# Kernel tuning notes

Measured on AMD Instinct MI355X. Metric: run time of the kernel, lower is better.

## Reference

```python
import jax, jax.numpy as jnp
import numpy as np

N_NODES = 100000

def gcn_layer(x, W, b, src, dst, norm):
    # x: [N, Fin], W: [Fin, Fout]; fused linear then normalized neighbor aggregation
    h = x @ W                                   # [N, Fout]
    msg = h[src] * norm[:, None]                # gather + per-edge scale, [E', Fout]
    agg = jax.ops.segment_sum(msg, dst, num_segments=N_NODES)  # scatter-add
    return agg + b

def _add_self_loops_and_norm(edge_index):
    src, dst = edge_index[0], edge_index[1]
    loop = jnp.arange(N_NODES, dtype=src.dtype)
    src = jnp.concatenate([src, loop])
    dst = jnp.concatenate([dst, loop])
    deg = jax.ops.segment_sum(jnp.ones_like(dst, dtype=jnp.float32), dst, num_segments=N_NODES)
    dis = jnp.where(deg > 0, jax.lax.rsqrt(deg), 0.0)   # deg^{-1/2}
    norm = dis[src] * dis[dst]                          # symmetric GCN normalization
    return src, dst, norm

def setup_inputs() -> dict:
    key = jax.random.key(0)
    k1, k2, k3, k4, k5, k6 = jax.random.split(key, 6)
    F_IN, F_HID, F_OUT = 64, 64, 64
    E = 1600000
    x = jax.random.normal(k1, (N_NODES, F_IN), dtype=jnp.float32)
    edge_index = jax.random.randint(k2, (2, E), 0, N_NODES, dtype=jnp.int64)
    s1 = 1.0 / np.sqrt(F_IN)
    s2 = 1.0 / np.sqrt(F_HID)
    W1 = jax.random.uniform(k3, (F_IN, F_HID), dtype=jnp.float32, minval=-s1, maxval=s1)
    b1 = jax.random.uniform(k4, (F_HID,), dtype=jnp.float32, minval=-s1, maxval=s1)
    W2 = jax.random.uniform(k5, (F_HID, F_OUT), dtype=jnp.float32, minval=-s2, maxval=s2)
    b2 = jax.random.uniform(k6, (F_OUT,), dtype=jnp.float32, minval=-s2, maxval=s2)
    return {"x": x, "edge_index": edge_index, "W1": W1, "b1": b1, "W2": W2, "b2": b2}

def reference(x, edge_index, W1, b1, W2, b2):
    src, dst, norm = _add_self_loops_and_norm(edge_index)
    h = gcn_layer(x, W1, b1, src, dst, norm)
    h = jax.nn.relu(h)
    h = gcn_layer(h, W2, b2, src, dst, norm)
    return h
```

## Files before the change

### kernel.cpp

```cpp
#include <hip/hip_runtime.h>
#include <cstdint>
#include <cstddef>


#define BK_SHIFT 9
#define BK_NODES 512
#define EPB 8192
#define CAP 12288
#define NBMAX 256

typedef short bf16x8 __attribute__((ext_vector_type(8)));
typedef float f32x4  __attribute__((ext_vector_type(4)));

static __device__ __forceinline__ unsigned short f2b(float f) {
    unsigned x = __float_as_uint(f);
    unsigned r = (x + 0x7FFFu + ((x >> 16) & 1u)) >> 16;
    return (unsigned short)r;
}
static __device__ __forceinline__ float blo(unsigned u) {
    return __uint_as_float(u << 16);
}
static __device__ __forceinline__ float bhi(unsigned u) {
    return __uint_as_float(u & 0xFFFF0000u);
}
static __device__ __forceinline__ void splitbf(float x, short& hi, short& lo) {
    unsigned short h = f2b(x);
    hi = (short)h;
    float r = x - __uint_as_float((unsigned)h << 16);
    lo = (short)f2b(r);
}

__global__ void k_init(int* __restrict__ gcursor, int NB) {
    int t = threadIdx.x;
    if (t < NB) gcursor[t] = t * CAP;
}

__global__ void __launch_bounds__(256) k_bscatter(const int* __restrict__ src,
                                                  const int* __restrict__ dst,
                                                  int* __restrict__ gcursor,
                                                  unsigned* __restrict__ packed,
                                                  int E, int NB) {
    __shared__ int hist[NBMAX];
    __shared__ int base[NBMAX];
    int t = threadIdx.x;
    for (int i = t; i < NB; i += 256) hist[i] = 0;
    __syncthreads();
    int e0 = blockIdx.x * EPB;
    int e1 = min(e0 + EPB, E);
    int4 dv[8];
    int kd[8];
#pragma unroll
    for (int k = 0; k < 8; ++k) {
        int e = e0 + t * 4 + k * 1024;
        kd[k] = (e + 3 < e1) ? 1 : 0;
        if (kd[k]) dv[k] = *(const int4*)(dst + e);
    }
#pragma unroll
    for (int k = 0; k < 8; ++k) {
        if (kd[k]) {
            atomicAdd(&hist[dv[k].x >> BK_SHIFT], 1);
            atomicAdd(&hist[dv[k].y >> BK_SHIFT], 1);
            atomicAdd(&hist[dv[k].z >> BK_SHIFT], 1);
            atomicAdd(&hist[dv[k].w >> BK_SHIFT], 1);
        }
    }
    __syncthreads();
    for (int i = t; i < NB; i += 256) {
        int c = hist[i];
        base[i] = c ? atomicAdd(&gcursor[i], c) : 0;
        hist[i] = 0;
    }
    __syncthreads();
    int4 sv[8];
#pragma unroll
    for (int k = 0; k < 8; ++k) {
        int e = e0 + t * 4 + k * 1024;
        if (kd[k]) sv[k] = *(const int4*)(src + e);
    }
#pragma unroll
    for (int k = 0; k < 8; ++k) {
        if (kd[k]) {
            int b0 = dv[k].x >> BK_SHIFT;
            int p0 = base[b0] + atomicAdd(&hist[b0], 1);
            packed[p0] = (unsigned)sv[k].x | (((unsigned)dv[k].x & (BK_NODES - 1)) << 17);
            int b1 = dv[k].y >> BK_SHIFT;
            int p1 = base[b1] + atomicAdd(&hist[b1], 1);
            packed[p1] = (unsigned)sv[k].y | (((unsigned)dv[k].y & (BK_NODES - 1)) << 17);
            int b2 = dv[k].z >> BK_SHIFT;
            int p2 = base[b2] + atomicAdd(&hist[b2], 1);
            packed[p2] = (unsigned)sv[k].z | (((unsigned)dv[k].z & (BK_NODES - 1)) << 17);
            int b3 = dv[k].w >> BK_SHIFT;
            int p3 = base[b3] + atomicAdd(&hist[b3], 1);
            packed[p3] = (unsigned)sv[k].w | (((unsigned)dv[k].w & (BK_NODES - 1)) << 17);
        }
    }
}

__global__ void __launch_bounds__(512) k_build(const unsigned* __restrict__ packed,
                                               const int* __restrict__ gcursor,
                                               int* __restrict__ rp,
                                               int* __restrict__ dega,
                                               float* __restrict__ dis,
                                               int* __restrict__ col, int N) {
    __shared__ int cnt_s[BK_NODES];
    __shared__ int tmp[BK_NODES];
    int b = blockIdx.x;
    int t = threadIdx.x;
    int node0 = b << BK_SHIFT;
    int nnode = min(BK_NODES, N - node0);
    int e0 = b * CAP;
    int e1 = gcursor[b];
    cnt_s[t] = 0;
    __syncthreads();
    for (int e = e0 + t * 4; e < e1; e += 2048) {
        int m = e1 - e; m = m > 4 ? 4 : m;
        unsigned p0 = packed[e];
        unsigned p1 = (m > 1) ? packed[e + 1] : 0;
        unsigned p2 = (m > 2) ? packed[e + 2] : 0;
        unsigned p3 = (m > 3) ? packed[e + 3] : 0;
        atomicAdd(&cnt_s[p0 >> 17], 1);
        if (m > 1) atomicAdd(&cnt_s[p1 >> 17], 1);
        if (m > 2) atomicAdd(&cnt_s[p2 >> 17], 1);
        if (m > 3) atomicAdd(&cnt_s[p3 >> 17], 1);
    }
    __syncthreads();
    int v = cnt_s[t];
    tmp[t] = v;
    __syncthreads();
    for (int off = 1; off < BK_NODES; off <<= 1) {
        int a = (t >= off) ? tmp[t - off] : 0;
        __syncthreads();
        tmp[t] += a;
        __syncthreads();
    }
    int excl = tmp[t] - v;
    if (t < nnode) {
        rp[node0 + t] = e0 + excl;
        dega[node0 + t] = v;
        dis[node0 + t] = rsqrtf((float)(v + 1));
    }
    __syncthreads();
    cnt_s[t] = excl;
    __syncthreads();
    for (int e = e0 + t * 4; e < e1; e += 2048) {
        int m = e1 - e; m = m > 4 ? 4 : m;
        unsigned p0 = packed[e];
        unsigned p1 = (m > 1) ? packed[e + 1] : 0;
        unsigned p2 = (m > 2) ? packed[e + 2] : 0;
        unsigned p3 = (m > 3) ? packed[e + 3] : 0;
        int pos0 = atomicAdd(&cnt_s[p0 >> 17], 1);
        col[e0 + pos0] = (int)(p0 & 0x1FFFFu);
        if (m > 1) { int pos = atomicAdd(&cnt_s[p1 >> 17], 1); col[e0 + pos] = (int)(p1 & 0x1FFFFu); }
        if (m > 2) { int pos = atomicAdd(&cnt_s[p2 >> 17], 1); col[e0 + pos] = (int)(p2 & 0x1FFFFu); }
        if (m > 3) { int pos = atomicAdd(&cnt_s[p3 >> 17], 1); col[e0 + pos] = (int)(p3 & 0x1FFFFu); }
    }
}

__global__ void __launch_bounds__(256) k_gemm_mfma(const float* __restrict__ X,
                                                   const float* __restrict__ W,
                                                   const float* __restrict__ dis,
                                                   unsigned short* __restrict__ g16,
                                                   int n, int nstrips) {
    __shared__ float Ws[4096];
    int t = threadIdx.x;
    {
        const float4* W4 = (const float4*)W;
        float4* S4 = (float4*)Ws;
#pragma unroll
        for (int i = 0; i < 4; ++i) S4[t + i * 256] = W4[t + i * 256];
    }
    __syncthreads();
    int wid  = t >> 6;
    int lane = t & 63;
    int quad = lane >> 4;
    int fl   = lane & 15;

    bf16x8 Bh[4][2], Bl[4][2];
#pragma unroll
    for (int tt = 0; tt < 4; ++tt)
#pragma unroll
        for (int c = 0; c < 2; ++c)
#pragma unroll
            for (int j = 0; j < 8; ++j) {
                float w = Ws[(c * 32 + quad * 8 + j) * 64 + tt * 16 + fl];
                short hi, lo;
                splitbf(w, hi, lo);
                Bh[tt][c][j] = hi;
                Bl[tt][c][j] = lo;
            }

    for (int s = blockIdx.x * 4 + wid; s < nstrips; s += gridDim.x * 4) {
        int row0 = s << 4;
        const float4* xp = (const float4*)(X + ((size_t)(row0 + fl) << 6));
        bf16x8 Ah[2], Al[2];
#pragma unroll
        for (int c = 0; c < 2; ++c) {
            float4 a = xp[c * 8 + quad * 2];
            float4 b = xp[c * 8 + quad * 2 + 1];
            float xs[8] = {a.x, a.y, a.z, a.w, b.x, b.y, b.z, b.w};
#pragma unroll
            for (int j = 0; j < 8; ++j) {
                short hi, lo;
                splitbf(xs[j], hi, lo);
                Ah[c][j] = hi;
                Al[c][j] = lo;
            }
        }
        f32x4 acc[4];
#pragma unroll
        for (int tt = 0; tt < 4; ++tt) acc[tt] = (f32x4){0.f, 0.f, 0.f, 0.f};
#pragma unroll
        for (int tt = 0; tt < 4; ++tt) {
#pragma unroll
            for (int c = 0; c < 2; ++c) {
                acc[tt] = __builtin_amdgcn_mfma_f32_16x16x32_bf16(Ah[c], Bh[tt][c], acc[tt], 0, 0, 0);
                acc[tt] = __builtin_amdgcn_mfma_f32_16x16x32_bf16(Al[c], Bh[tt][c], acc[tt], 0, 0, 0);
                acc[tt] = __builtin_amdgcn_mfma_f32_16x16x32_bf16(Ah[c], Bl[tt][c], acc[tt], 0, 0, 0);
            }
        }
        float4 dv = *(const float4*)(dis + row0 + quad * 4);
        float ds4[4] = {dv.x, dv.y, dv.z, dv.w};
#pragma unroll
        for (int tt = 0; tt < 4; ++tt) {
#pragma unroll
            for (int r = 0; r < 4; ++r) {
                int row = row0 + quad * 4 + r;
                float v = acc[tt][r] * ds4[r];
                g16[(size_t)row * 64 + tt * 16 + fl] = f2b(v);
            }
        }
    }
}

template <int RELU>
__global__ void __launch_bounds__(256) k_agg(const unsigned short* __restrict__ g16,
                                             const int* __restrict__ col,
                                             const int* __restrict__ rp,
                                             const int* __restrict__ dega,
                                             const float* __restrict__ dis,
                                             const float* __restrict__ bias,
                                             float* __restrict__ out, int n) {
    int lane = threadIdx.x & 63;
    int wv = (blockIdx.x << 2) | (threadIdx.x >> 6);
    int sub = lane >> 3;
    int fl  = lane & 7;
    int base = wv << 3;
    if (base >= n) return;
    int node = base + sub;
    int nd = min(node, n - 1);
    int start = rp[nd];
    int deg = (node < n) ? dega[nd] : 0;
    int dm = max(deg, __shfl_xor(deg, 8));
    dm = max(dm, __shfl_xor(dm, 16));
    dm = max(dm, __shfl_xor(dm, 32));

    uint4 us = *((const uint4*)(g16 + ((size_t)nd << 6)) + fl);
    float A[8], B[8], C[8], D[8];
    A[0] = blo(us.x); A[1] = bhi(us.x); A[2] = blo(us.y); A[3] = bhi(us.y);
    A[4] = blo(us.z); A[5] = bhi(us.z); A[6] = blo(us.w); A[7] = bhi(us.w);
#pragma unroll
    for (int j = 0; j < 8; ++j) { B[j] = 0.f; C[j] = 0.f; D[j] = 0.f; }

    int sb = sub << 3;
    for (int c = 0; c < dm; c += 8) {
        int rem = deg - c;
        int cv = 0;
        if (fl < rem) cv = col[start + c + fl];
        int rr[8];
#pragma unroll
        for (int i = 0; i < 8; ++i) rr[i] = __shfl(cv, sb + i);
        uint4 u[8];
#pragma unroll
        for (int i = 0; i < 8; ++i)
            if (i < rem) u[i] = *((const uint4*)(g16 + ((size_t)rr[i] << 6)) + fl);
#pragma unroll
        for (int i = 0; i < 8; ++i) {
            if (i < rem) {
                float* T = ((i & 3) == 0) ? A : ((i & 3) == 1) ? B : ((i & 3) == 2) ? C : D;
                T[0] += blo(u[i].x); T[1] += bhi(u[i].x);
                T[2] += blo(u[i].y); T[3] += bhi(u[i].y);
                T[4] += blo(u[i].z); T[5] += bhi(u[i].z);
                T[6] += blo(u[i].w); T[7] += bhi(u[i].w);
            }
        }
    }
    float s = dis[nd];
    float4 bv0 = ((const float4*)bias)[fl * 2];
    float4 bv1 = ((const float4*)bias)[fl * 2 + 1];
    float r[8];
#pragma unroll
    for (int j = 0; j < 8; ++j) r[j] = (A[j] + B[j]) + (C[j] + D[j]);
    float4 o0, o1;
    o0.x = fmaf(s, r[0], bv0.x); o0.y = fmaf(s, r[1], bv0.y);
    o0.z = fmaf(s, r[2], bv0.z); o0.w = fmaf(s, r[3], bv0.w);
    o1.x = fmaf(s, r[4], bv1.x); o1.y = fmaf(s, r[5], bv1.y);
    o1.z = fmaf(s, r[6], bv1.z); o1.w = fmaf(s, r[7], bv1.w);
    if (RELU) {
        o0.x = fmaxf(o0.x, 0.f); o0.y = fmaxf(o0.y, 0.f);
        o0.z = fmaxf(o0.z, 0.f); o0.w = fmaxf(o0.w, 0.f);
        o1.x = fmaxf(o1.x, 0.f); o1.y = fmaxf(o1.y, 0.f);
        o1.z = fmaxf(o1.z, 0.f); o1.w = fmaxf(o1.w, 0.f);
    }
    if (node < n) {
        float4* op = (float4*)(out + ((size_t)node << 6)) + fl * 2;
        op[0] = o0;
        op[1] = o1;
    }
}

extern "C" void kernel_launch(void* const* d_in, const int* in_sizes, int n_in,
                              void* d_out, int out_size, void* d_ws, size_t ws_size,
                              hipStream_t stream) {
    const float* x  = (const float*)d_in[0];
    const int*   ei = (const int*)d_in[1];
    const float* W1 = (const float*)d_in[2];
    const float* b1 = (const float*)d_in[3];
    const float* W2 = (const float*)d_in[4];
    const float* b2 = (const float*)d_in[5];
    float* out = (float*)d_out;

    const int N = in_sizes[0] / 64;
    const int E = in_sizes[1] / 2;
    const int NB = (N + BK_NODES - 1) >> BK_SHIFT;
    const int nstrips = (N + 15) >> 4;
    const int* src = ei;
    const int* dst = ei + E;

    char* ws = (char*)d_ws;
    size_t off = 0;
    auto alloc = [&](size_t bytes) -> void* {
        void* p = ws + off;
        off = (off + bytes + 255) & ~(size_t)255;
        return p;
    };
    int*            gcursor = (int*)alloc((size_t)NB * 4);
    int*            rp      = (int*)alloc((size_t)N * 4);
    int*            dega    = (int*)alloc((size_t)N * 4);
    float*          dis     = (float*)alloc((size_t)N * 4);
    unsigned*       packed  = (unsigned*)alloc((size_t)NB * CAP * 4);
    int*            col     = (int*)alloc((size_t)NB * CAP * 4);
    unsigned short* g16     = (unsigned short*)alloc((size_t)N * 64 * 2);
    float*          h       = (float*)alloc((size_t)N * 64 * 4);
    (void)ws_size;

    k_init<<<1, 256, 0, stream>>>(gcursor, NB);
    k_bscatter<<<(E + EPB - 1) / EPB, 256, 0, stream>>>(src, dst, gcursor, packed, E, NB);
    k_build<<<NB, 512, 0, stream>>>(packed, gcursor, rp, dega, dis, col, N);

    k_gemm_mfma<<<782, 256, 0, stream>>>(x, W1, dis, g16, N, nstrips);
    k_agg<1><<<(N + 31) / 32, 256, 0, stream>>>(g16, col, rp, dega, dis, b1, h, N);
    k_gemm_mfma<<<782, 256, 0, stream>>>(h, W2, dis, g16, N, nstrips);
    k_agg<0><<<(N + 31) / 32, 256, 0, stream>>>(g16, col, rp, dega, dis, b2, out, N);
}
```

Measured before the change: 205.2 us.

## Fuse layer-1 aggregation with layer-2 linear transform in one kernel

Adds a kernel that aggregates layer-1 neighbor features, applies bias and ReLU, then multiplies by W2 held in shared memory using wavefront shuffles. It writes the bf16 layer-2 features directly, removing the fp32 hidden buffer round-trip and one kernel launch. In exchange, the MFMA GEMM for layer 2 becomes scalar FMA work with 64 shuffles per node, which adds ALU and latency cost to the aggregation kernel.

```diff
diff --git a/kernel.cpp b/kernel.cpp
--- a/kernel.cpp
+++ b/kernel.cpp
@@ -308,6 +308,116 @@
     }
 }
 
+__global__ void __launch_bounds__(256) k_agg_gemm(const unsigned short* __restrict__ g16,
+                                                  const int* __restrict__ col,
+                                                  const int* __restrict__ rp,
+                                                  const int* __restrict__ dega,
+                                                  const float* __restrict__ dis,
+                                                  const float* __restrict__ bias,
+                                                  const float* __restrict__ W2,
+                                                  unsigned short* __restrict__ g16out,
+                                                  int n) {
+    __shared__ float W2s[4096];
+    int t = threadIdx.x;
+    {
+        const float4* W4 = (const float4*)W2;
+        float4* S4 = (float4*)W2s;
+#pragma unroll
+        for (int i = 0; i < 4; ++i) S4[t + i * 256] = W4[t + i * 256];
+    }
+    __syncthreads();
+
+    int lane = t & 63;
+    int wv = (blockIdx.x << 2) | (t >> 6);
+    int sub = lane >> 3;
+    int fl  = lane & 7;
+    int base = wv << 3;
+    if (base >= n) return;
+    int node = base + sub;
+    int nd = min(node, n - 1);
+    int start = rp[nd];
+    int deg = (node < n) ? dega[nd] : 0;
+    int dm = max(deg, __shfl_xor(deg, 8));
+    dm = max(dm, __shfl_xor(dm, 16));
+    dm = max(dm, __shfl_xor(dm, 32));
+
+    uint4 us = *((const uint4*)(g16 + ((size_t)nd << 6)) + fl);
+    float A[8], B[8], C[8], D[8];
+    A[0] = blo(us.x); A[1] = bhi(us.x); A[2] = blo(us.y); A[3] = bhi(us.y);
+    A[4] = blo(us.z); A[5] = bhi(us.z); A[6] = blo(us.w); A[7] = bhi(us.w);
+#pragma unroll
+    for (int j = 0; j < 8; ++j) { B[j] = 0.f; C[j] = 0.f; D[j] = 0.f; }
+
+    int sb = sub << 3;
+    for (int c = 0; c < dm; c += 8) {
+        int rem = deg - c;
+        int cv = 0;
+        if (fl < rem) cv = col[start + c + fl];
+        int rr[8];
+#pragma unroll
+        for (int i = 0; i < 8; ++i) rr[i] = __shfl(cv, sb + i);
+        uint4 u[8];
+#pragma unroll
+        for (int i = 0; i < 8; ++i)
+            if (i < rem) u[i] = *((const uint4*)(g16 + ((size_t)rr[i] << 6)) + fl);
+#pragma unroll
+        for (int i = 0; i < 8; ++i) {
+            if (i < rem) {
+                float* T = ((i & 3) == 0) ? A : ((i & 3) == 1) ? B : ((i & 3) == 2) ? C : D;
+                T[0] += blo(u[i].x); T[1] += bhi(u[i].x);
+                T[2] += blo(u[i].y); T[3] += bhi(u[i].y);
+                T[4] += blo(u[i].z); T[5] += bhi(u[i].z);
+                T[6] += blo(u[i].w); T[7] += bhi(u[i].w);
+            }
+        }
+    }
+    float s = dis[nd];
+    float4 bv0 = ((const float4*)bias)[fl * 2];
+    float4 bv1 = ((const float4*)bias)[fl * 2 + 1];
+    float r[8];
+#pragma unroll
+    for (int j = 0; j < 8; ++j) r[j] = (A[j] + B[j]) + (C[j] + D[j]);
+    r[0] = fmaxf(fmaf(s, r[0], bv0.x), 0.f);
+    r[1] = fmaxf(fmaf(s, r[1], bv0.y), 0.f);
+    r[2] = fmaxf(fmaf(s, r[2], bv0.z), 0.f);
+    r[3] = fmaxf(fmaf(s, r[3], bv0.w), 0.f);
+    r[4] = fmaxf(fmaf(s, r[4], bv1.x), 0.f);
+    r[5] = fmaxf(fmaf(s, r[5], bv1.y), 0.f);
+    r[6] = fmaxf(fmaf(s, r[6], bv1.z), 0.f);
+    r[7] = fmaxf(fmaf(s, r[7], bv1.w), 0.f);
+
+    float acc[8];
+#pragma unroll
+    for (int j = 0; j < 8; ++j) acc[j] = 0.f;
+#pragma unroll
+    for (int g = 0; g < 8; ++g) {
+        float hk[8];
+#pragma unroll
+        for (int q = 0; q < 8; ++q) hk[q] = __shfl(r[q], sb + g);
+#pragma unroll
+        for (int q = 0; q < 8; ++q) {
+            const float4* wp = (const float4*)&W2s[(g * 8 + q) * 64 + fl * 8];
+            float4 wa = wp[0], wb = wp[1];
+            acc[0] = fmaf(hk[q], wa.x, acc[0]);
+            acc[1] = fmaf(hk[q], wa.y, acc[1]);
+            acc[2] = fmaf(hk[q], wa.z, acc[2]);
+            acc[3] = fmaf(hk[q], wa.w, acc[3]);
+            acc[4] = fmaf(hk[q], wb.x, acc[4]);
+            acc[5] = fmaf(hk[q], wb.y, acc[5]);
+            acc[6] = fmaf(hk[q], wb.z, acc[6]);
+            acc[7] = fmaf(hk[q], wb.w, acc[7]);
+        }
+    }
+    if (node < n) {
+        uint4 o;
+        o.x = (unsigned)f2b(acc[0] * s) | ((unsigned)f2b(acc[1] * s) << 16);
+        o.y = (unsigned)f2b(acc[2] * s) | ((unsigned)f2b(acc[3] * s) << 16);
+        o.z = (unsigned)f2b(acc[4] * s) | ((unsigned)f2b(acc[5] * s) << 16);
+        o.w = (unsigned)f2b(acc[6] * s) | ((unsigned)f2b(acc[7] * s) << 16);
+        *((uint4*)(g16out + ((size_t)node << 6)) + fl) = o;
+    }
+}
+
 extern "C" void kernel_launch(void* const* d_in, const int* in_sizes, int n_in,
                               void* d_out, int out_size, void* d_ws, size_t ws_size,
                               hipStream_t stream) {
@@ -340,7 +450,7 @@
     unsigned*       packed  = (unsigned*)alloc((size_t)NB * CAP * 4);
     int*            col     = (int*)alloc((size_t)NB * CAP * 4);
     unsigned short* g16     = (unsigned short*)alloc((size_t)N * 64 * 2);
-    float*          h       = (float*)alloc((size_t)N * 64 * 4);
+    unsigned short* g16b    = (unsigned short*)alloc((size_t)N * 64 * 2);
     (void)ws_size;
 
     k_init<<<1, 256, 0, stream>>>(gcursor, NB);
@@ -348,7 +458,6 @@
     k_build<<<NB, 512, 0, stream>>>(packed, gcursor, rp, dega, dis, col, N);
 
     k_gemm_mfma<<<782, 256, 0, stream>>>(x, W1, dis, g16, N, nstrips);
-    k_agg<1><<<(N + 31) / 32, 256, 0, stream>>>(g16, col, rp, dega, dis, b1, h, N);
-    k_gemm_mfma<<<782, 256, 0, stream>>>(h, W2, dis, g16, N, nstrips);
-    k_agg<0><<<(N + 31) / 32, 256, 0, stream>>>(g16, col, rp, dega, dis, b2, out, N);
-}
+    k_agg_gemm<<<(N + 31) / 32, 256, 0, stream>>>(g16, col, rp, dega, dis, b1, W2, g16b, N);
+    k_agg<0><<<(N + 31) / 32, 256, 0, stream>>>(g16b, col, rp, dega, dis, b2, out, N);
+}
```

New measurement: 255.9 us. 24.7% more time.

## Double-buffer neighbor gathers in aggregation kernel to overlap loads with accumulation

Applied to the files above, without the earlier changes.

Restructures the CSR aggregation loop so the next chunk of 8 neighbor-row gathers is issued before the current chunk is accumulated, using two register buffers in a software pipeline. To pay for the extra buffer registers, the accumulator sets drop from four to two, and launch bounds now ask for 4 blocks per CU. The aim is to hide global gather latency by keeping more loads in flight per wave. The risk is register pressure from two 8-entry uint4 buffers, which could cause spills or lower occupancy.

```diff
diff --git a/kernel.cpp b/kernel.cpp
--- a/kernel.cpp
+++ b/kernel.cpp
@@ -233,13 +233,13 @@
 }
 
 template <int RELU>
-__global__ void __launch_bounds__(256) k_agg(const unsigned short* __restrict__ g16,
-                                             const int* __restrict__ col,
-                                             const int* __restrict__ rp,
-                                             const int* __restrict__ dega,
-                                             const float* __restrict__ dis,
-                                             const float* __restrict__ bias,
-                                             float* __restrict__ out, int n) {
+__global__ void __launch_bounds__(256, 4) k_agg(const unsigned short* __restrict__ g16,
+                                                const int* __restrict__ col,
+                                                const int* __restrict__ rp,
+                                                const int* __restrict__ dega,
+                                                const float* __restrict__ dis,
+                                                const float* __restrict__ bias,
+                                                float* __restrict__ out, int n) {
     int lane = threadIdx.x & 63;
     int wv = (blockIdx.x << 2) | (threadIdx.x >> 6);
     int sub = lane >> 3;
@@ -255,41 +255,54 @@
     dm = max(dm, __shfl_xor(dm, 32));
 
     uint4 us = *((const uint4*)(g16 + ((size_t)nd << 6)) + fl);
-    float A[8], B[8], C[8], D[8];
+    float A[8], B[8];
     A[0] = blo(us.x); A[1] = bhi(us.x); A[2] = blo(us.y); A[3] = bhi(us.y);
     A[4] = blo(us.z); A[5] = bhi(us.z); A[6] = blo(us.w); A[7] = bhi(us.w);
 #pragma unroll
-    for (int j = 0; j < 8; ++j) { B[j] = 0.f; C[j] = 0.f; D[j] = 0.f; }
+    for (int j = 0; j < 8; ++j) B[j] = 0.f;
 
     int sb = sub << 3;
-    for (int c = 0; c < dm; c += 8) {
-        int rem = deg - c;
+    uint4 u0[8], u1[8];
+
+    auto ISSUE = [&](uint4* u, int c) {
+        int r = deg - c;
         int cv = 0;
-        if (fl < rem) cv = col[start + c + fl];
+        if (fl < r) cv = col[start + c + fl];
         int rr[8];
 #pragma unroll
         for (int i = 0; i < 8; ++i) rr[i] = __shfl(cv, sb + i);
-        uint4 u[8];
 #pragma unroll
         for (int i = 0; i < 8; ++i)
-            if (i < rem) u[i] = *((const uint4*)(g16 + ((size_t)rr[i] << 6)) + fl);
+            if (i < r) u[i] = *((const uint4*)(g16 + ((size_t)rr[i] << 6)) + fl);
+    };
+    auto ACCUM = [&](const uint4* u, int c) {
+        int r = deg - c;
 #pragma unroll
         for (int i = 0; i < 8; ++i) {
-            if (i < rem) {
-                float* T = ((i & 3) == 0) ? A : ((i & 3) == 1) ? B : ((i & 3) == 2) ? C : D;
+            if (i < r) {
+                float* T = (i & 1) ? B : A;
                 T[0] += blo(u[i].x); T[1] += bhi(u[i].x);
                 T[2] += blo(u[i].y); T[3] += bhi(u[i].y);
                 T[4] += blo(u[i].z); T[5] += bhi(u[i].z);
                 T[6] += blo(u[i].w); T[7] += bhi(u[i].w);
             }
         }
-    }
+    };
+
+    ISSUE(u0, 0);
+    for (int c = 0; c < dm; c += 16) {
+        if (c + 8 < dm) ISSUE(u1, c + 8);
+        ACCUM(u0, c);
+        if (c + 16 < dm) ISSUE(u0, c + 16);
+        if (c + 8 < dm) ACCUM(u1, c + 8);
+    }
+
     float s = dis[nd];
     float4 bv0 = ((const float4*)bias)[fl * 2];
     float4 bv1 = ((const float4*)bias)[fl * 2 + 1];
     float r[8];
 #pragma unroll
-    for (int j = 0; j < 8; ++j) r[j] = (A[j] + B[j]) + (C[j] + D[j]);
+    for (int j = 0; j < 8; ++j) r[j] = A[j] + B[j];
     float4 o0, o1;
     o0.x = fmaf(s, r[0], bv0.x); o0.y = fmaf(s, r[1], bv0.y);
     o0.z = fmaf(s, r[2], bv0.z); o0.w = fmaf(s, r[3], bv0.w);
```

After: 208.4 us. Within noise of the previous version (+1.5%).
